# Kernel tuning notes

Hardware: AMD Instinct MI355X
Metric: run time of the kernel (lower is better)

## Reference

```python
import jax, jax.numpy as jnp
import numpy as np

B, N, C = 16, 577, 768
H = 12
D = C // H
HID = C // 2
TEMP_MIN, TEMP_MAX = 0.5, 3.0


def setup_inputs() -> dict:
    key = jax.random.key(0)
    ks = jax.random.split(key, 8)
    s = 0.02
    return {
        "x": jax.random.normal(ks[0], (B, N, C), dtype=jnp.float32),
        "qkv_w": jax.random.normal(ks[1], (C, 3 * C), dtype=jnp.float32) * s,
        "proj_w": jax.random.normal(ks[2], (C, C), dtype=jnp.float32) * s,
        "proj_b": jnp.zeros((C,), dtype=jnp.float32),
        "t_w1": jax.random.normal(ks[3], (C, HID), dtype=jnp.float32) * s,
        "t_b1": jnp.zeros((HID,), dtype=jnp.float32),
        "t_w2": jax.random.normal(ks[4], (HID, 1), dtype=jnp.float32) * s,
        "t_b2": jnp.zeros((1,), dtype=jnp.float32),
    }


def reference(x, qkv_w, proj_w, proj_b, t_w1, t_b1, t_w2, t_b2):
    b, n, c = x.shape
    scale = D ** -0.5
    # instance-wise temperature from CLS token: (B, 1)
    cls = x[:, 0]
    h = jax.nn.relu(cls @ t_w1 + t_b1)
    t_norm = jax.nn.sigmoid(h @ t_w2 + t_b2)
    temperature = TEMP_MIN + (TEMP_MAX - TEMP_MIN) * t_norm  # (B, 1)

    qkv = (x @ qkv_w).reshape(b, n, 3, H, D)
    q = qkv[:, :, 0].transpose(0, 2, 1, 3)  # (B, H, N, D)
    k = qkv[:, :, 1].transpose(0, 2, 1, 3)
    v = qkv[:, :, 2].transpose(0, 2, 1, 3)

    attn = jnp.einsum('bhqd,bhkd->bhqk', q, k) * scale
    attn = attn / temperature[:, :, None, None]  # (B,1,1,1) broadcast
    attn = jax.nn.softmax(attn, axis=-1)
    out = jnp.einsum('bhqk,bhkd->bhqd', attn, v)
    out = out.transpose(0, 2, 1, 3).reshape(b, n, c)
    return out @ proj_w + proj_b
```

## Files before the change

kernel.cpp:

```cpp
#include <hip/hip_runtime.h>
#include <hip/hip_bf16.h>
#include <stdint.h>

typedef unsigned short u16;
typedef unsigned int   u32;
typedef uint64_t       u64;

using f32x4  = __attribute__((ext_vector_type(4))) float;
using bf16x8 = __attribute__((ext_vector_type(8))) short;

__device__ __forceinline__ u16 f2bf(float f){
  u32 x = __builtin_bit_cast(u32, f);
  x = x + 0x7fffu + ((x >> 16) & 1u);
  return (u16)(x >> 16);
}

__device__ __forceinline__ void gload16(const void* g, void* l){
  __builtin_amdgcn_global_load_lds(
      (const __attribute__((address_space(1))) void*)g,
      (__attribute__((address_space(3))) void*)l, 16, 0, 0);
}

__device__ __forceinline__ bf16x8 mkfrag(uint2 h0, uint2 h1){
  union { bf16x8 v; u32 u[4]; } f;
  f.u[0]=h0.x; f.u[1]=h0.y; f.u[2]=h1.x; f.u[3]=h1.y;
  return f.v;
}

__global__ void convx(const float* __restrict__ in, u16* __restrict__ out, int n4){
  for (int i = blockIdx.x*256 + threadIdx.x; i < n4; i += gridDim.x*256){
    float4 v = ((const float4*)in)[i];
    ushort4 o;
    o.x = f2bf(v.x); o.y = f2bf(v.y); o.z = f2bf(v.z); o.w = f2bf(v.w);
    ((ushort4*)out)[i] = o;
  }
}

__global__ __launch_bounds__(256) void wtrans(const float* __restrict__ in,
                                              u16* __restrict__ out, int K, int N){
  __shared__ float tile[32][33];
  const int t = threadIdx.x;
  const int n0 = blockIdx.x*32, k0 = blockIdx.y*32;
  const int r = t >> 3, c4 = (t & 7)*4;
  const float4 v = *(const float4*)(in + (u64)(k0 + r)*N + n0 + c4);
  tile[r][c4+0]=v.x; tile[r][c4+1]=v.y; tile[r][c4+2]=v.z; tile[r][c4+3]=v.w;
  __syncthreads();
  ushort4 o;
  o.x = f2bf(tile[c4+0][r]); o.y = f2bf(tile[c4+1][r]);
  o.z = f2bf(tile[c4+2][r]); o.w = f2bf(tile[c4+3][r]);
  *(ushort4*)(out + (u64)(n0 + r)*K + k0 + c4) = o;
}

__global__ __launch_bounds__(384) void temp_kernel(
    const float* __restrict__ x, const float* __restrict__ w1,
    const float* __restrict__ b1, const float* __restrict__ w2,
    const float* __restrict__ b2, float* __restrict__ lsc){
  const int b = blockIdx.x, t = threadIdx.x;
  __shared__ float cls[768];
  __shared__ float part[6];
  const float* xr = x + (u64)b*577*768;
  cls[t] = xr[t]; cls[t+384] = xr[t+384];
  __syncthreads();
  float h0 = 0.f, h1 = 0.f, h2 = 0.f, h3 = 0.f;
  for (int i = 0; i < 768; i += 4){
    h0 = fmaf(cls[i+0], w1[(u64)(i+0)*384 + t], h0);
    h1 = fmaf(cls[i+1], w1[(u64)(i+1)*384 + t], h1);
    h2 = fmaf(cls[i+2], w1[(u64)(i+2)*384 + t], h2);
    h3 = fmaf(cls[i+3], w1[(u64)(i+3)*384 + t], h3);
  }
  float hacc = fmaxf((h0 + h1) + (h2 + h3) + b1[t], 0.f);
  float v = hacc * w2[t];
  #pragma unroll
  for (int off = 1; off < 64; off <<= 1) v += __shfl_xor(v, off);
  if ((t & 63) == 0) part[t >> 6] = v;
  __syncthreads();
  if (t == 0){
    float s2 = b2[0];
    for (int i = 0; i < 6; i++) s2 += part[i];
    float sig  = 1.f / (1.f + expf(-s2));
    float temp = 0.5f + 2.5f * sig;
    lsc[b] = 0.125f / temp;
  }
}

template<int OUTF>
__global__ __launch_bounds__(256, 2) void gemm_nt(
    const u16* __restrict__ A, const u16* __restrict__ Bm,
    void* __restrict__ Cout, const float* __restrict__ bias, int M, int N){
  constexpr int K = 768;
  __shared__ u16 As[128*64];
  __shared__ u16 Bs[128*64];
  const int t = threadIdx.x, l = t & 63, w = t >> 6;
  const int bm = blockIdx.y*128, bn = blockIdx.x*128;
  const int wr = (w >> 1)*64, wc = (w & 1)*64;
  const int g = l >> 4, r16 = l & 15;

  f32x4 acc[4][4];
  #pragma unroll
  for (int i = 0; i < 4; i++)
    #pragma unroll
    for (int j = 0; j < 4; j++) acc[i][j] = (f32x4){0.f,0.f,0.f,0.f};

  const int srow = t >> 3;
  const int su   = (t & 7) ^ (srow & 7);
  const u16* gA[4]; const u16* gB[4];
  #pragma unroll
  for (int i = 0; i < 4; i++){
    int ra = bm + i*32 + srow; if (ra > M-1) ra = M-1;
    gA[i] = A  + (u64)ra*K + su*8;
    gB[i] = Bm + (u64)(bn + i*32 + srow)*K + su*8;
  }
  u16* lA = As + t*8;
  u16* lB = Bs + t*8;

  for (int kt = 0; kt < K; kt += 64){
    #pragma unroll
    for (int i = 0; i < 4; i++) gload16(gA[i] + kt, lA + i*2048);
    #pragma unroll
    for (int i = 0; i < 4; i++) gload16(gB[i] + kt, lB + i*2048);
    __syncthreads();
    #pragma unroll
    for (int s = 0; s < 2; s++){
      const int c   = s*4 + (g >> 1);
      const int off = (g & 1)*4;
      bf16x8 af[4], bfr[4];
      #pragma unroll
      for (int m = 0; m < 4; m++){
        const int R = wr + m*16 + r16;
        const int i1 = R*64 + ((c ^ (R & 7))*8) + off;
        af[m] = mkfrag(*(const uint2*)(As + i1), *(const uint2*)(As + (i1 ^ 16)));
      }
      #pragma unroll
      for (int n = 0; n < 4; n++){
        const int R = wc + n*16 + r16;
        const int i1 = R*64 + ((c ^ (R & 7))*8) + off;
        bfr[n] = mkfrag(*(const uint2*)(Bs + i1), *(const uint2*)(Bs + (i1 ^ 16)));
      }
      #pragma unroll
      for (int m = 0; m < 4; m++)
        #pragma unroll
        for (int n = 0; n < 4; n++)
          acc[m][n] = __builtin_amdgcn_mfma_f32_16x16x32_bf16(af[m], bfr[n], acc[m][n], 0, 0, 0);
    }
    __syncthreads();
  }
  const int row0 = bm + wr + g*4;
  const int col0 = bn + wc + r16;
  #pragma unroll
  for (int m = 0; m < 4; m++){
    #pragma unroll
    for (int rr = 0; rr < 4; rr++){
      const int row = row0 + m*16 + rr;
      if (row < M){
        #pragma unroll
        for (int n = 0; n < 4; n++){
          const int col = col0 + n*16;
          const float v = acc[m][n][rr];
          if (OUTF) ((float*)Cout)[(u64)row*N + col] = v + bias[col];
          else      ((u16*)Cout)[(u64)row*N + col]  = f2bf(v);
        }
      }
    }
  }
}

__global__ __launch_bounds__(256, 2) void attn_kernel(
    const u16* __restrict__ qkv, const float* __restrict__ lsc_arr,
    u16* __restrict__ aout){
  const int qt = blockIdx.x, h = blockIdx.y, b = blockIdx.z;
  const int t = threadIdx.x, w = t >> 6, l = t & 63;
  const int g = l >> 4, r16 = l & 15;
  __shared__ u16 Ks[64*64];
  __shared__ u16 Vt[64*64];
  const float lscale = lsc_arr[b];
  const u16* base = qkv + (u64)b*577*2304 + (u64)h*64;

  int qn = qt*64 + w*16 + r16; if (qn > 576) qn = 576;
  bf16x8 qf[2];
  {
    const u16* qr = base + (u64)qn*2304;
    #pragma unroll
    for (int s = 0; s < 2; s++)
      qf[s] = mkfrag(*(const uint2*)(qr + s*32 + g*4),
                     *(const uint2*)(qr + s*32 + g*4 + 16));
  }
  float m_run = -1e30f, l_run = 0.f;
  f32x4 oacc[4];
  #pragma unroll
  for (int i = 0; i < 4; i++) oacc[i] = (f32x4){0,0,0,0};

  const u16* kg = base + 768;
  const u16* vg = base + 1536;
  const int srcb = (l & 48) | (((l >> 4) & 3)*4);

  for (int kt = 0; kt < 10; kt++){
    #pragma unroll
    for (int i = 0; i < 2; i++){
      const int kr = i*32 + (t >> 3);
      int kn = kt*64 + kr; if (kn > 576) kn = 576;
      uint4 kv = *(const uint4*)(kg + (u64)kn*2304 + (t & 7)*8);
      *(uint4*)(Ks + kr*64 + (((t & 7) ^ (kr & 7))*8)) = kv;
    }
    {
      const int kr0 = (t >> 3)*2;
      int kn0 = kt*64 + kr0, kn1 = kn0 + 1;
      if (kn0 > 576) kn0 = 576;
      if (kn1 > 576) kn1 = 576;
      uint4 r0 = *(const uint4*)(vg + (u64)kn0*2304 + (t & 7)*8);
      uint4 r1 = *(const uint4*)(vg + (u64)kn1*2304 + (t & 7)*8);
      const u16* e0 = (const u16*)&r0;
      const u16* e1 = (const u16*)&r1;
      #pragma unroll
      for (int j = 0; j < 8; j++){
        const int d = (t & 7)*8 + j;
        const int key = (d ^ (d >> 3)) & 7;
        const u32 val = (u32)e0[j] | ((u32)e1[j] << 16);
        *(u32*)(Vt + d*64 + (((kr0 >> 3) ^ key)*8) + (kr0 & 7)) = val;
      }
    }
    __syncthreads();

    f32x4 sacc[4];
    #pragma unroll
    for (int i = 0; i < 4; i++) sacc[i] = (f32x4){0,0,0,0};
    #pragma unroll
    for (int fn = 0; fn < 4; fn++){
      const int kr = fn*16 + r16;
      const int kk = kr & 7;
      const u16* rowp = Ks + kr*64 + (g & 1)*4;
      #pragma unroll
      for (int s = 0; s < 2; s++){
        const int b0 = (4*s + (g >> 1)) ^ kk;
        sacc[fn] = __builtin_amdgcn_mfma_f32_16x16x32_bf16(
            mkfrag(*(const uint2*)(rowp + b0*8), *(const uint2*)(rowp + (b0 ^ 2)*8)),
            qf[s], sacc[fn], 0, 0, 0);
      }
    }
    #pragma unroll
    for (int fn = 0; fn < 4; fn++)
      #pragma unroll
      for (int rr = 0; rr < 4; rr++){
        const bool valid = (kt*64 + fn*16 + g*4 + rr) <= 576;
        const float v = sacc[fn][rr]*lscale;
        sacc[fn][rr] = valid ? v : -1e30f;
      }
    float mx = sacc[0][0];
    #pragma unroll
    for (int fn = 0; fn < 4; fn++)
      #pragma unroll
      for (int rr = 0; rr < 4; rr++) mx = fmaxf(mx, sacc[fn][rr]);
    mx = fmaxf(mx, __shfl_xor(mx, 16));
    mx = fmaxf(mx, __shfl_xor(mx, 32));
    const float nm = fmaxf(m_run, mx);
    const float corr = __expf(m_run - nm);
    m_run = nm;
    float rs = 0.f;
    u16 pb[4][4];
    #pragma unroll
    for (int fn = 0; fn < 4; fn++)
      #pragma unroll
      for (int rr = 0; rr < 4; rr++){
        const float p = __expf(sacc[fn][rr] - m_run);
        rs += p;
        pb[fn][rr] = f2bf(p);
      }
    rs += __shfl_xor(rs, 16);
    rs += __shfl_xor(rs, 32);
    l_run = l_run*corr + rs;
    float corrO[4];
    #pragma unroll
    for (int rr = 0; rr < 4; rr++) corrO[rr] = __shfl(corr, srcb + rr);
    #pragma unroll
    for (int df = 0; df < 4; df++)
      #pragma unroll
      for (int rr = 0; rr < 4; rr++)
        oacc[df][rr] *= corrO[rr];
    #pragma unroll
    for (int s = 0; s < 2; s++){
      union { bf16x8 v; u32 u[4]; } pa;
      pa.u[0] = (u32)pb[2*s][0]   | ((u32)pb[2*s][1]   << 16);
      pa.u[1] = (u32)pb[2*s][2]   | ((u32)pb[2*s][3]   << 16);
      pa.u[2] = (u32)pb[2*s+1][0] | ((u32)pb[2*s+1][1] << 16);
      pa.u[3] = (u32)pb[2*s+1][2] | ((u32)pb[2*s+1][3] << 16);
      #pragma unroll
      for (int df = 0; df < 4; df++){
        const int vd = df*16 + r16;
        const int vk = (vd ^ (vd >> 3)) & 7;
        const u16* vrp = Vt + vd*64 + (g & 1)*4;
        const int c0 = (4*s + (g >> 1)) ^ vk;
        const bf16x8 vf = mkfrag(*(const uint2*)(vrp + c0*8),
                                 *(const uint2*)(vrp + (c0 ^ 2)*8));
        oacc[df] = __builtin_amdgcn_mfma_f32_16x16x32_bf16(pa.v, vf, oacc[df], 0, 0, 0);
      }
    }
    __syncthreads();
  }
  float lO[4];
  #pragma unroll
  for (int rr = 0; rr < 4; rr++) lO[rr] = __shfl(l_run, srcb + rr);
  #pragma unroll
  for (int df = 0; df < 4; df++){
    const int d = df*16 + r16;
    #pragma unroll
    for (int rr = 0; rr < 4; rr++){
      const int n = qt*64 + w*16 + g*4 + rr;
      if (n <= 576){
        const float v = oacc[df][rr] / lO[rr];
        aout[(u64)(b*577 + n)*768 + h*64 + d] = f2bf(v);
      }
    }
  }
}

extern "C" void kernel_launch(void* const* d_in, const int* in_sizes, int n_in,
                              void* d_out, int out_size, void* d_ws, size_t ws_size,
                              hipStream_t stream){
  const float* x      = (const float*)d_in[0];
  const float* qkv_w  = (const float*)d_in[1];
  const float* proj_w = (const float*)d_in[2];
  const float* proj_b = (const float*)d_in[3];
  const float* t_w1   = (const float*)d_in[4];
  const float* t_b1   = (const float*)d_in[5];
  const float* t_w2   = (const float*)d_in[6];
  const float* t_b2   = (const float*)d_in[7];

  const u64 off_xb  = 256;
  const u64 off_qwT = off_xb  + 14180352ull;
  const u64 off_pwT = off_qwT + 3538944ull;
  const u64 off_qkv = off_pwT + 1179648ull;
  const u64 off_ao  = off_qkv + 42541056ull;
  const u64 need    = off_ao  + 14180352ull;
  if (ws_size < need) return;

  char* ws  = (char*)d_ws;
  float* lsc = (float*)ws;
  u16* xb   = (u16*)(ws + off_xb);
  u16* qwT  = (u16*)(ws + off_qwT);
  u16* pwT  = (u16*)(ws + off_pwT);
  u16* qkv  = (u16*)(ws + off_qkv);
  u16* ao   = (u16*)(ws + off_ao);

  convx<<<1024, 256, 0, stream>>>(x, xb, (16*577*768)/4);
  wtrans<<<dim3(2304/32, 768/32), 256, 0, stream>>>(qkv_w, qwT, 768, 2304);
  wtrans<<<dim3(768/32, 768/32), 256, 0, stream>>>(proj_w, pwT, 768, 768);
  temp_kernel<<<16, 384, 0, stream>>>(x, t_w1, t_b1, t_w2, t_b2, lsc);
  gemm_nt<0><<<dim3(2304/128, 73), 256, 0, stream>>>(xb, qwT, qkv, nullptr, 9232, 2304);
  attn_kernel<<<dim3(10, 12, 16), 256, 0, stream>>>(qkv, lsc, ao);
  gemm_nt<1><<<dim3(768/128, 73), 256, 0, stream>>>(ao, pwT, d_out, proj_b, 9232, 768);
}
```

Measured before the change: 253.3 us.

## Double-buffer K/V tiles in attention and fold softmax scale into Q

Attention now double-buffers K and V tiles in LDS, loading K asynchronously straight into shared memory and prefetching V into registers while the current tile is computed. This replaces the serial load-sync-compute pattern with one barrier per tile. The temperature/softmax scale is applied to Q in the QKV GEMM epilogue, and score masking runs only on the final tile. Index clamping is removed, so out-of-range key rows read neighbouring data that the mask must neutralise. The attention output reuses the bf16 x buffer.

```diff
diff --git a/kernel.cpp b/kernel.cpp
--- a/kernel.cpp
+++ b/kernel.cpp
@@ -86,7 +86,8 @@
 template<int OUTF>
 __global__ __launch_bounds__(256, 2) void gemm_nt(
     const u16* __restrict__ A, const u16* __restrict__ Bm,
-    void* __restrict__ Cout, const float* __restrict__ bias, int M, int N){
+    void* __restrict__ Cout, const float* __restrict__ bias,
+    const float* __restrict__ lsc, int M, int N){
   constexpr int K = 768;
   __shared__ u16 As[128*64];
   __shared__ u16 Bs[128*64];
@@ -146,18 +147,21 @@
   }
   const int row0 = bm + wr + g*4;
   const int col0 = bn + wc + r16;
+  const bool isQ = (OUTF == 2) && (bn < 768);
   #pragma unroll
   for (int m = 0; m < 4; m++){
     #pragma unroll
     for (int rr = 0; rr < 4; rr++){
       const int row = row0 + m*16 + rr;
       if (row < M){
+        float qs = 1.0f;
+        if (isQ) qs = lsc[row/577];
         #pragma unroll
         for (int n = 0; n < 4; n++){
           const int col = col0 + n*16;
           const float v = acc[m][n][rr];
-          if (OUTF) ((float*)Cout)[(u64)row*N + col] = v + bias[col];
-          else      ((u16*)Cout)[(u64)row*N + col]  = f2bf(v);
+          if (OUTF == 1) ((float*)Cout)[(u64)row*N + col] = v + bias[col];
+          else           ((u16*)Cout)[(u64)row*N + col]  = f2bf(v*qs);
         }
       }
     }
@@ -165,14 +169,12 @@
 }
 
 __global__ __launch_bounds__(256, 2) void attn_kernel(
-    const u16* __restrict__ qkv, const float* __restrict__ lsc_arr,
-    u16* __restrict__ aout){
+    const u16* __restrict__ qkv, u16* __restrict__ aout){
   const int qt = blockIdx.x, h = blockIdx.y, b = blockIdx.z;
   const int t = threadIdx.x, w = t >> 6, l = t & 63;
   const int g = l >> 4, r16 = l & 15;
-  __shared__ u16 Ks[64*64];
-  __shared__ u16 Vt[64*64];
-  const float lscale = lsc_arr[b];
+  __shared__ u16 Ks[2][64*64];
+  __shared__ u16 Vt[2][64*64];
   const u16* base = qkv + (u64)b*577*2304 + (u64)h*64;
 
   int qn = qt*64 + w*16 + r16; if (qn > 576) qn = 576;
@@ -189,36 +191,47 @@
   #pragma unroll
   for (int i = 0; i < 4; i++) oacc[i] = (f32x4){0,0,0,0};
 
-  const u16* kg = base + 768;
-  const u16* vg = base + 1536;
   const int srcb = (l & 48) | (((l >> 4) & 3)*4);
 
+  const int srow = t >> 3;
+  const int su   = (t & 7) ^ (srow & 7);
+  const u16* pK = base + 768  + (u64)srow*2304 + su*8;
+  const int kr0 = (t >> 3)*2;
+  const u16* pV = base + 1536 + (u64)kr0*2304 + (t & 7)*8;
+  u32 vtoff[8];
+  #pragma unroll
+  for (int j = 0; j < 8; j++){
+    const int d = (t & 7)*8 + j;
+    const int key = (d ^ (d >> 3)) & 7;
+    vtoff[j] = d*64 + (((kr0 >> 3) ^ key)*8) + (kr0 & 7);
+  }
+
+  uint4 vr0, vr1;
+  gload16(pK,            &Ks[0][0] + t*8);
+  gload16(pK + 32*2304,  &Ks[0][0] + t*8 + 2048);
+  vr0 = *(const uint4*)pV;
+  vr1 = *(const uint4*)(pV + 2304);
+  pK += 64*2304; pV += 64*2304;
+  {
+    const u16* e0 = (const u16*)&vr0;
+    const u16* e1 = (const u16*)&vr1;
+    #pragma unroll
+    for (int j = 0; j < 8; j++)
+      *(u32*)(&Vt[0][0] + vtoff[j]) = (u32)e0[j] | ((u32)e1[j] << 16);
+  }
+  __syncthreads();
+
   for (int kt = 0; kt < 10; kt++){
-    #pragma unroll
-    for (int i = 0; i < 2; i++){
-      const int kr = i*32 + (t >> 3);
-      int kn = kt*64 + kr; if (kn > 576) kn = 576;
-      uint4 kv = *(const uint4*)(kg + (u64)kn*2304 + (t & 7)*8);
-      *(uint4*)(Ks + kr*64 + (((t & 7) ^ (kr & 7))*8)) = kv;
-    }
-    {
-      const int kr0 = (t >> 3)*2;
-      int kn0 = kt*64 + kr0, kn1 = kn0 + 1;
-      if (kn0 > 576) kn0 = 576;
-      if (kn1 > 576) kn1 = 576;
-      uint4 r0 = *(const uint4*)(vg + (u64)kn0*2304 + (t & 7)*8);
-      uint4 r1 = *(const uint4*)(vg + (u64)kn1*2304 + (t & 7)*8);
-      const u16* e0 = (const u16*)&r0;
-      const u16* e1 = (const u16*)&r1;
-      #pragma unroll
-      for (int j = 0; j < 8; j++){
-        const int d = (t & 7)*8 + j;
-        const int key = (d ^ (d >> 3)) & 7;
-        const u32 val = (u32)e0[j] | ((u32)e1[j] << 16);
-        *(u32*)(Vt + d*64 + (((kr0 >> 3) ^ key)*8) + (kr0 & 7)) = val;
-      }
-    }
-    __syncthreads();
+    const int cur = kt & 1, nb = cur ^ 1;
+    u16* ksc = &Ks[cur][0];
+    u16* vtc = &Vt[cur][0];
+    if (kt < 9){
+      gload16(pK,           &Ks[nb][0] + t*8);
+      gload16(pK + 32*2304, &Ks[nb][0] + t*8 + 2048);
+      vr0 = *(const uint4*)pV;
+      vr1 = *(const uint4*)(pV + 2304);
+      pK += 64*2304; pV += 64*2304;
+    }
 
     f32x4 sacc[4];
     #pragma unroll
@@ -227,7 +240,7 @@
     for (int fn = 0; fn < 4; fn++){
       const int kr = fn*16 + r16;
       const int kk = kr & 7;
-      const u16* rowp = Ks + kr*64 + (g & 1)*4;
+      const u16* rowp = ksc + kr*64 + (g & 1)*4;
       #pragma unroll
       for (int s = 0; s < 2; s++){
         const int b0 = (4*s + (g >> 1)) ^ kk;
@@ -236,14 +249,15 @@
             qf[s], sacc[fn], 0, 0, 0);
       }
     }
-    #pragma unroll
-    for (int fn = 0; fn < 4; fn++)
-      #pragma unroll
-      for (int rr = 0; rr < 4; rr++){
-        const bool valid = (kt*64 + fn*16 + g*4 + rr) <= 576;
-        const float v = sacc[fn][rr]*lscale;
-        sacc[fn][rr] = valid ? v : -1e30f;
-      }
+    if (kt == 9){
+      #pragma unroll
+      for (int fn = 0; fn < 4; fn++)
+        #pragma unroll
+        for (int rr = 0; rr < 4; rr++){
+          const bool valid = (576 + fn*16 + g*4 + rr) <= 576;
+          sacc[fn][rr] = valid ? sacc[fn][rr] : -1e30f;
+        }
+    }
     float mx = sacc[0][0];
     #pragma unroll
     for (int fn = 0; fn < 4; fn++)
@@ -286,12 +300,20 @@
       for (int df = 0; df < 4; df++){
         const int vd = df*16 + r16;
         const int vk = (vd ^ (vd >> 3)) & 7;
-        const u16* vrp = Vt + vd*64 + (g & 1)*4;
+        const u16* vrp = vtc + vd*64 + (g & 1)*4;
         const int c0 = (4*s + (g >> 1)) ^ vk;
         const bf16x8 vf = mkfrag(*(const uint2*)(vrp + c0*8),
                                  *(const uint2*)(vrp + (c0 ^ 2)*8));
         oacc[df] = __builtin_amdgcn_mfma_f32_16x16x32_bf16(pa.v, vf, oacc[df], 0, 0, 0);
       }
+    }
+    if (kt < 9){
+      const u16* e0 = (const u16*)&vr0;
+      const u16* e1 = (const u16*)&vr1;
+      u16* vtn = &Vt[nb][0];
+      #pragma unroll
+      for (int j = 0; j < 8; j++)
+        *(u32*)(vtn + vtoff[j]) = (u32)e0[j] | ((u32)e1[j] << 16);
     }
     __syncthreads();
   }
@@ -328,8 +350,7 @@
   const u64 off_qwT = off_xb  + 14180352ull;
   const u64 off_pwT = off_qwT + 3538944ull;
   const u64 off_qkv = off_pwT + 1179648ull;
-  const u64 off_ao  = off_qkv + 42541056ull;
-  const u64 need    = off_ao  + 14180352ull;
+  const u64 need    = off_qkv + 42835968ull;
   if (ws_size < need) return;
 
   char* ws  = (char*)d_ws;
@@ -338,13 +359,13 @@
   u16* qwT  = (u16*)(ws + off_qwT);
   u16* pwT  = (u16*)(ws + off_pwT);
   u16* qkv  = (u16*)(ws + off_qkv);
-  u16* ao   = (u16*)(ws + off_ao);
+  u16* ao   = xb;
 
   convx<<<1024, 256, 0, stream>>>(x, xb, (16*577*768)/4);
   wtrans<<<dim3(2304/32, 768/32), 256, 0, stream>>>(qkv_w, qwT, 768, 2304);
   wtrans<<<dim3(768/32, 768/32), 256, 0, stream>>>(proj_w, pwT, 768, 768);
   temp_kernel<<<16, 384, 0, stream>>>(x, t_w1, t_b1, t_w2, t_b2, lsc);
-  gemm_nt<0><<<dim3(2304/128, 73), 256, 0, stream>>>(xb, qwT, qkv, nullptr, 9232, 2304);
-  attn_kernel<<<dim3(10, 12, 16), 256, 0, stream>>>(qkv, lsc, ao);
-  gemm_nt<1><<<dim3(768/128, 73), 256, 0, stream>>>(ao, pwT, d_out, proj_b, 9232, 768);
-}
+  gemm_nt<2><<<dim3(2304/128, 73), 256, 0, stream>>>(xb, qwT, qkv, nullptr, lsc, 9232, 2304);
+  attn_kernel<<<dim3(10, 12, 16), 256, 0, stream>>>(qkv, ao);
+  gemm_nt<1><<<dim3(768/128, 73), 256, 0, stream>>>(ao, pwT, d_out, proj_b, nullptr, 9232, 768);
+}
```

Result: no change. 255.1 us (+0.7%).
